# Kernel tuning notes

Measured on AMD Instinct MI355X. Metric: run time of the kernel, lower is better.

## Reference

```python
import jax, jax.numpy as jnp
import numpy as np

B, S, D, R, H = 32, 2048, 512, 4, 32  # batch, seq, input_dim, num_regimes, gru hidden

def setup_inputs() -> dict:
    key = jax.random.key(0)
    ks = jax.random.split(key, 16)
    def lin(k, fan_out, fan_in):
        s = 1.0 / np.sqrt(fan_in)
        kw, kb = jax.random.split(k)
        return (jax.random.uniform(kw, (fan_out, fan_in), jnp.float32, -s, s),
                jax.random.uniform(kb, (fan_out,), jnp.float32, -s, s))
    x = jax.random.normal(ks[0], (B, S, D), jnp.float32)
    rw1, rb1 = lin(ks[1], 128, D)
    rw2, rb2 = lin(ks[2], 64, 128)
    rw3, rb3 = lin(ks[3], R, 64)
    # experts stacked: [R, out, in]
    e1 = [lin(jax.random.fold_in(ks[4], i), 64, D) for i in range(R)]
    e2 = [lin(jax.random.fold_in(ks[5], i), 64, 64) for i in range(R)]
    ew1 = jnp.stack([w for w, _ in e1]); eb1 = jnp.stack([b for _, b in e1])
    ew2 = jnp.stack([w for w, _ in e2]); eb2 = jnp.stack([b for _, b in e2])
    sg = 1.0 / np.sqrt(H)
    gw_ih = jax.random.uniform(ks[6], (3 * H, R), jnp.float32, -sg, sg)
    gw_hh = jax.random.uniform(ks[7], (3 * H, H), jnp.float32, -sg, sg)
    gb_ih = jax.random.uniform(ks[8], (3 * H,), jnp.float32, -sg, sg)
    gb_hh = jax.random.uniform(ks[9], (3 * H,), jnp.float32, -sg, sg)
    return dict(x=x, rw1=rw1, rb1=rb1, rw2=rw2, rb2=rb2, rw3=rw3, rb3=rb3,
                ew1=ew1, eb1=eb1, ew2=ew2, eb2=eb2,
                gw_ih=gw_ih, gw_hh=gw_hh, gb_ih=gb_ih, gb_hh=gb_hh)

def reference(x, rw1, rb1, rw2, rb2, rw3, rb3, ew1, eb1, ew2, eb2, gw_ih, gw_hh, gb_ih, gb_hh):
    # --- router (dropout is identity in eval) ---
    h = jax.nn.relu(jnp.einsum('bsd,fd->bsf', x, rw1) + rb1)
    h = jax.nn.relu(jnp.einsum('bsf,gf->bsg', h, rw2) + rb2)
    probs = jax.nn.softmax(jnp.einsum('bsg,rg->bsr', h, rw3) + rb3, axis=-1)  # [B,S,R]
    # --- batched experts: one fused batched-GEMM instead of a python loop ---
    e = jax.nn.relu(jnp.einsum('bsd,red->bsre', x, ew1) + eb1)      # [B,S,R,64]
    e = jax.nn.relu(jnp.einsum('bsre,rfe->bsrf', e, ew2) + eb2)     # [B,S,R,64]
    weighted = jnp.einsum('bsrf,bsr->bsf', e, probs)                 # [B,S,64]
    # --- GRU over regime probs (pytorch gate ordering r,z,n) ---
    def step(hprev, xt):
        gi = xt @ gw_ih.T + gb_ih    # [B,3H]
        gh = hprev @ gw_hh.T + gb_hh
        ir, iz, inn = jnp.split(gi, 3, axis=-1)
        hr, hz, hn = jnp.split(gh, 3, axis=-1)
        r = jax.nn.sigmoid(ir + hr)
        z = jax.nn.sigmoid(iz + hz)
        n = jnp.tanh(inn + r * hn)
        hnew = (1.0 - z) * n + z * hprev
        return hnew, hnew
    h0 = jnp.zeros((probs.shape[0], gw_hh.shape[1]), probs.dtype)
    _, trans = jax.lax.scan(step, h0, jnp.swapaxes(probs, 0, 1))
    trans = jnp.swapaxes(trans, 0, 1)  # [B,S,H]
    uncertainty = jnp.std(probs, axis=-1, ddof=1)  # torch.std is unbiased
    return probs, weighted, trans, uncertainty
```

## Files before the change

### kernel.cpp

```cpp
#include <hip/hip_runtime.h>
#include <math.h>

#define NTOK 65536
#define TOK 64
#define NTILE 1024

__device__ __forceinline__ float xhalf_sum(float a) {
    unsigned ai = __builtin_bit_cast(unsigned, a);
    auto r = __builtin_amdgcn_permlane32_swap(ai, ai, false, false);
    return __builtin_bit_cast(float, (unsigned)r[0]) +
           __builtin_bit_cast(float, (unsigned)r[1]);
}

__global__ __launch_bounds__(256, 2) void k_router(
    const float* __restrict__ x,
    const float* __restrict__ rw1, const float* __restrict__ rb1,
    const float* __restrict__ rw2, const float* __restrict__ rb2,
    const float* __restrict__ rw3, const float* __restrict__ rb3,
    float* __restrict__ probs_out, float* __restrict__ unc_out)
{
    __shared__ float XsT[32][68];
    __shared__ float WsT[32][132];
    __shared__ float H1[64][132];
    __shared__ float H2[64][68];

    const int tid = threadIdx.x;
    const int tx = tid & 15, ty = tid >> 4;
    const long t0 = (long)blockIdx.x * TOK;

    float acc[4][8];
#pragma unroll
    for (int i = 0; i < 4; i++)
#pragma unroll
        for (int o = 0; o < 8; o++) acc[i][o] = 0.f;

    for (int kc = 0; kc < 16; kc++) {
        __syncthreads();
#pragma unroll
        for (int s = 0; s < 2; s++) {
            int id = tid + s * 256;
            int tok = id >> 3, kq = id & 7;
            float4 v = *(const float4*)&x[(t0 + tok) * 512 + kc * 32 + kq * 4];
            XsT[kq * 4 + 0][tok] = v.x; XsT[kq * 4 + 1][tok] = v.y;
            XsT[kq * 4 + 2][tok] = v.z; XsT[kq * 4 + 3][tok] = v.w;
        }
#pragma unroll
        for (int s = 0; s < 4; s++) {
            int id = tid + s * 256;
            int out = id >> 3, kq = id & 7;
            float4 v = *(const float4*)&rw1[(long)out * 512 + kc * 32 + kq * 4];
            WsT[kq * 4 + 0][out] = v.x; WsT[kq * 4 + 1][out] = v.y;
            WsT[kq * 4 + 2][out] = v.z; WsT[kq * 4 + 3][out] = v.w;
        }
        __syncthreads();
#pragma unroll
        for (int k = 0; k < 32; k++) {
            const float4 xv = *(const float4*)&XsT[k][ty * 4];
            const float4 wa = *(const float4*)&WsT[k][tx * 4];
            const float4 wb = *(const float4*)&WsT[k][64 + tx * 4];
            const float xs[4] = {xv.x, xv.y, xv.z, xv.w};
            const float ws[8] = {wa.x, wa.y, wa.z, wa.w, wb.x, wb.y, wb.z, wb.w};
#pragma unroll
            for (int i = 0; i < 4; i++)
#pragma unroll
                for (int o = 0; o < 8; o++)
                    acc[i][o] = fmaf(xs[i], ws[o], acc[i][o]);
        }
    }

#pragma unroll
    for (int o = 0; o < 8; o++) {
        const int col = (o < 4) ? (tx * 4 + o) : (64 + tx * 4 + (o - 4));
        float b = rb1[col];
#pragma unroll
        for (int i = 0; i < 4; i++) {
            float v = acc[i][o] + b;
            H1[ty * 4 + i][col] = v > 0.f ? v : 0.f;
        }
    }
    __syncthreads();

    float a2[4][4];
#pragma unroll
    for (int i = 0; i < 4; i++)
#pragma unroll
        for (int o = 0; o < 4; o++) a2[i][o] = 0.f;

    for (int k4 = 0; k4 < 32; k4++) {
        float4 hv[4], wv[4];
#pragma unroll
        for (int i = 0; i < 4; i++) hv[i] = *(const float4*)&H1[ty * 4 + i][k4 * 4];
#pragma unroll
        for (int o = 0; o < 4; o++) wv[o] = *(const float4*)&rw2[(tx * 4 + o) * 128 + k4 * 4];
#pragma unroll
        for (int i = 0; i < 4; i++)
#pragma unroll
            for (int o = 0; o < 4; o++)
                a2[i][o] += hv[i].x * wv[o].x + hv[i].y * wv[o].y +
                            hv[i].z * wv[o].z + hv[i].w * wv[o].w;
    }
#pragma unroll
    for (int o = 0; o < 4; o++) {
        float b = rb2[tx * 4 + o];
#pragma unroll
        for (int i = 0; i < 4; i++) {
            float v = a2[i][o] + b;
            H2[ty * 4 + i][tx * 4 + o] = v > 0.f ? v : 0.f;
        }
    }
    __syncthreads();

    if (tid < 64) {
        int tok = tid;
        float lg[4];
#pragma unroll
        for (int r = 0; r < 4; r++) {
            float s = rb3[r];
            for (int k4 = 0; k4 < 16; k4++) {
                float4 h = *(const float4*)&H2[tok][k4 * 4];
                float4 w = *(const float4*)&rw3[r * 64 + k4 * 4];
                s += h.x * w.x + h.y * w.y + h.z * w.z + h.w * w.w;
            }
            lg[r] = s;
        }
        float m = fmaxf(fmaxf(lg[0], lg[1]), fmaxf(lg[2], lg[3]));
        float e0 = __expf(lg[0] - m), e1 = __expf(lg[1] - m);
        float e2 = __expf(lg[2] - m), e3 = __expf(lg[3] - m);
        float inv = __builtin_amdgcn_rcpf(e0 + e1 + e2 + e3);
        float p0 = e0 * inv, p1 = e1 * inv, p2 = e2 * inv, p3 = e3 * inv;
        *(float4*)&probs_out[(t0 + tok) * 4] = make_float4(p0, p1, p2, p3);
        float mean = 0.25f * (p0 + p1 + p2 + p3);
        float d0 = p0 - mean, d1 = p1 - mean, d2 = p2 - mean, d3 = p3 - mean;
        unc_out[t0 + tok] = sqrtf((d0 * d0 + d1 * d1 + d2 * d2 + d3 * d3) * (1.f / 3.f));
    }
}

__global__ __launch_bounds__(256, 2) void k_experts_gru(
    const float* __restrict__ x,
    const float* __restrict__ ew1, const float* __restrict__ eb1,
    const float* __restrict__ ew2, const float* __restrict__ eb2,
    const float* __restrict__ probs, float* __restrict__ weighted_out,
    const float* __restrict__ gwih, const float* __restrict__ gwhh,
    const float* __restrict__ gbih, const float* __restrict__ gbhh,
    float* __restrict__ trans_out)
{
    if (blockIdx.x < 32) {
        if (threadIdx.x >= 64) return;
        const int b = blockIdx.x;
        const int l = threadIdx.x;
        const int j = l & 31, half = l >> 5;
        __shared__ __align__(16) float hS[32];

        float whh[3][16];
#pragma unroll
        for (int g = 0; g < 3; g++) {
            const float* wp = gwhh + (j + 32 * g) * 32 + half * 16;
#pragma unroll
            for (int q = 0; q < 4; q++) {
                float4 w = *(const float4*)(wp + q * 4);
                whh[g][q * 4 + 0] = w.x; whh[g][q * 4 + 1] = w.y;
                whh[g][q * 4 + 2] = w.z; whh[g][q * 4 + 3] = w.w;
            }
        }
        float wih[3][4];
#pragma unroll
        for (int g = 0; g < 3; g++) {
            float4 w = *(const float4*)&gwih[(j + 32 * g) * 4];
            wih[g][0] = w.x; wih[g][1] = w.y; wih[g][2] = w.z; wih[g][3] = w.w;
        }
        const float bR = gbih[j] + gbhh[j];
        const float bZ = gbih[j + 32] + gbhh[j + 32];
        const float bIN = gbih[j + 64], bHN = gbhh[j + 64];

        const float* pb = probs + (long)b * 2048 * 4;
        float4 p0 = *(const float4*)pb;
        float4 p1 = *(const float4*)(pb + 4);
        float hk[16];
#pragma unroll
        for (int k = 0; k < 16; k++) hk[k] = 0.f;
        float hj = 0.f;
        float* tr = trans_out + (long)b * 2048 * 32 + j;

        for (int t = 0; t < 2048; t++) {
            const int tn = (t + 2 < 2048) ? (t + 2) : 2047;
            float4 p2 = *(const float4*)(pb + tn * 4);

            float aR0 = 0.f, aR1 = 0.f, aZ0 = 0.f, aZ1 = 0.f, aN0 = 0.f, aN1 = 0.f;
#pragma unroll
            for (int k = 0; k < 16; k += 2) {
                aR0 = fmaf(whh[0][k],     hk[k],     aR0);
                aR1 = fmaf(whh[0][k + 1], hk[k + 1], aR1);
                aZ0 = fmaf(whh[1][k],     hk[k],     aZ0);
                aZ1 = fmaf(whh[1][k + 1], hk[k + 1], aZ1);
                aN0 = fmaf(whh[2][k],     hk[k],     aN0);
                aN1 = fmaf(whh[2][k + 1], hk[k + 1], aN1);
            }
            float aR = xhalf_sum(aR0 + aR1);
            float aZ = xhalf_sum(aZ0 + aZ1);
            float aN = xhalf_sum(aN0 + aN1);

            float giR = fmaf(wih[0][3], p0.w, fmaf(wih[0][2], p0.z,
                        fmaf(wih[0][1], p0.y, fmaf(wih[0][0], p0.x, bR))));
            float giZ = fmaf(wih[1][3], p0.w, fmaf(wih[1][2], p0.z,
                        fmaf(wih[1][1], p0.y, fmaf(wih[1][0], p0.x, bZ))));
            float giN = fmaf(wih[2][3], p0.w, fmaf(wih[2][2], p0.z,
                        fmaf(wih[2][1], p0.y, fmaf(wih[2][0], p0.x, bIN))));

            float r = __builtin_amdgcn_rcpf(1.f + __expf(-(giR + aR)));
            float z = __builtin_amdgcn_rcpf(1.f + __expf(-(giZ + aZ)));
            float nx = giN + r * (aN + bHN);
            float n = fmaf(2.f, __builtin_amdgcn_rcpf(1.f + __expf(-2.f * nx)), -1.f);
            hj = fmaf(z, hj - n, n);

            if (l < 32) tr[t * 32] = hj;
            hS[j] = hj;
            asm volatile("s_waitcnt lgkmcnt(0)" ::: "memory");
#pragma unroll
            for (int q = 0; q < 4; q++) {
                float4 h4 = *(const float4*)&hS[half * 16 + q * 4];
                hk[q * 4 + 0] = h4.x; hk[q * 4 + 1] = h4.y;
                hk[q * 4 + 2] = h4.z; hk[q * 4 + 3] = h4.w;
            }
            p0 = p1; p1 = p2;
        }
        return;
    }

    __shared__ float XsT[32][68];
    __shared__ float WsT[32][132];
    __shared__ float E1[64][132];
    __shared__ float pS[64][4];

    const int tid = threadIdx.x;
    const int tx = tid & 15, ty = tid >> 4;
    const long t0 = (long)(blockIdx.x - 32) * TOK;

    if (tid < 64) *(float4*)&pS[tid][0] = *(const float4*)&probs[(t0 + tid) * 4];

    float wacc[4][8];
#pragma unroll
    for (int i = 0; i < 4; i++)
#pragma unroll
        for (int o = 0; o < 8; o++) wacc[i][o] = 0.f;

    for (int g = 0; g < 2; g++) {
        float acc[4][8];
#pragma unroll
        for (int i = 0; i < 4; i++)
#pragma unroll
            for (int o = 0; o < 8; o++) acc[i][o] = 0.f;

        for (int kc = 0; kc < 16; kc++) {
            __syncthreads();
#pragma unroll
            for (int s = 0; s < 2; s++) {
                int id = tid + s * 256;
                int tok = id >> 3, kq = id & 7;
                float4 v = *(const float4*)&x[(t0 + tok) * 512 + kc * 32 + kq * 4];
                XsT[kq * 4 + 0][tok] = v.x; XsT[kq * 4 + 1][tok] = v.y;
                XsT[kq * 4 + 2][tok] = v.z; XsT[kq * 4 + 3][tok] = v.w;
            }
#pragma unroll
            for (int s = 0; s < 4; s++) {
                int id = tid + s * 256;
                int out = id >> 3, kq = id & 7;
                float4 v = *(const float4*)&ew1[(long)(g * 128 + out) * 512 + kc * 32 + kq * 4];
                WsT[kq * 4 + 0][out] = v.x; WsT[kq * 4 + 1][out] = v.y;
                WsT[kq * 4 + 2][out] = v.z; WsT[kq * 4 + 3][out] = v.w;
            }
            __syncthreads();
#pragma unroll
            for (int k = 0; k < 32; k++) {
                const float4 xv = *(const float4*)&XsT[k][ty * 4];
                const float4 wa = *(const float4*)&WsT[k][tx * 4];
                const float4 wb = *(const float4*)&WsT[k][64 + tx * 4];
                const float xs[4] = {xv.x, xv.y, xv.z, xv.w};
                const float ws[8] = {wa.x, wa.y, wa.z, wa.w, wb.x, wb.y, wb.z, wb.w};
#pragma unroll
                for (int i = 0; i < 4; i++)
#pragma unroll
                    for (int o = 0; o < 8; o++)
                        acc[i][o] = fmaf(xs[i], ws[o], acc[i][o]);
            }
        }
        __syncthreads();
#pragma unroll
        for (int o = 0; o < 8; o++) {
            const int col = (o < 4) ? (tx * 4 + o) : (64 + tx * 4 + (o - 4));
            float b = eb1[g * 128 + col];
#pragma unroll
            for (int i = 0; i < 4; i++) {
                float v = acc[i][o] + b;
                E1[ty * 4 + i][col] = v > 0.f ? v : 0.f;
            }
        }
        __syncthreads();

        const int rl = tx >> 3;
        const int fb = (tx & 7) * 8;
        const int rg = g * 2 + rl;

        float a2[4][8];
#pragma unroll
        for (int i = 0; i < 4; i++)
#pragma unroll
            for (int o = 0; o < 8; o++) a2[i][o] = 0.f;

        for (int k4 = 0; k4 < 16; k4++) {
            float4 hv[4];
#pragma unroll
            for (int i = 0; i < 4; i++)
                hv[i] = *(const float4*)&E1[ty * 4 + i][rl * 64 + k4 * 4];
#pragma unroll
            for (int o = 0; o < 8; o++) {
                float4 wv = *(const float4*)&ew2[(long)(rg * 64 + fb + o) * 64 + k4 * 4];
#pragma unroll
                for (int i = 0; i < 4; i++)
                    a2[i][o] += hv[i].x * wv.x + hv[i].y * wv.y +
                                hv[i].z * wv.z + hv[i].w * wv.w;
            }
        }
        float pr[4];
#pragma unroll
        for (int i = 0; i < 4; i++) pr[i] = pS[ty * 4 + i][rg];
#pragma unroll
        for (int o = 0; o < 8; o++) {
            float b = eb2[rg * 64 + fb + o];
#pragma unroll
            for (int i = 0; i < 4; i++) {
                float v = a2[i][o] + b;
                v = v > 0.f ? v : 0.f;
                wacc[i][o] = fmaf(pr[i], v, wacc[i][o]);
            }
        }
        __syncthreads();
    }

#pragma unroll
    for (int i = 0; i < 4; i++)
#pragma unroll
        for (int o = 0; o < 8; o++)
            wacc[i][o] += __shfl_xor(wacc[i][o], 8);

    if ((tx & 8) == 0) {
#pragma unroll
        for (int i = 0; i < 4; i++) {
            float4 v0 = make_float4(wacc[i][0], wacc[i][1], wacc[i][2], wacc[i][3]);
            float4 v1 = make_float4(wacc[i][4], wacc[i][5], wacc[i][6], wacc[i][7]);
            long base = (t0 + ty * 4 + i) * 64 + (tx & 7) * 8;
            *(float4*)&weighted_out[base] = v0;
            *(float4*)&weighted_out[base + 4] = v1;
        }
    }
}

extern "C" void kernel_launch(void* const* d_in, const int* in_sizes, int n_in,
                              void* d_out, int out_size, void* d_ws, size_t ws_size,
                              hipStream_t stream) {
    const float* x    = (const float*)d_in[0];
    const float* rw1  = (const float*)d_in[1];
    const float* rb1  = (const float*)d_in[2];
    const float* rw2  = (const float*)d_in[3];
    const float* rb2  = (const float*)d_in[4];
    const float* rw3  = (const float*)d_in[5];
    const float* rb3  = (const float*)d_in[6];
    const float* ew1  = (const float*)d_in[7];
    const float* eb1  = (const float*)d_in[8];
    const float* ew2  = (const float*)d_in[9];
    const float* eb2  = (const float*)d_in[10];
    const float* gwih = (const float*)d_in[11];
    const float* gwhh = (const float*)d_in[12];
    const float* gbih = (const float*)d_in[13];
    const float* gbhh = (const float*)d_in[14];

    float* out        = (float*)d_out;
    float* probs_o    = out;
    float* weighted_o = out + 262144;
    float* trans_o    = out + 262144 + 4194304;
    float* unc_o      = trans_o + 2097152;

    hipLaunchKernelGGL(k_router, dim3(NTILE), dim3(256), 0, stream,
                       x, rw1, rb1, rw2, rb2, rw3, rb3, probs_o, unc_o);
    hipLaunchKernelGGL(k_experts_gru, dim3(NTILE + 32), dim3(256), 0, stream,
                       x, ew1, eb1, ew2, eb2, probs_o, weighted_o,
                       gwih, gwhh, gbih, gbhh, trans_o);
}
```

Measured before the change: 829.7 us.

## Fuse router, experts and GRU into one kernel with per-tile flag handoff

Merges the router and experts/GRU kernels into a single persistent-style launch. Each token tile computes router probs, keeps them in shared memory for the expert stage, and publishes a release flag. The 32 GRU blocks spin on these flags per 64-step chunk, so the sequential recurrence can overlap the router/expert GEMMs instead of waiting for a full kernel boundary. Tiles are remapped so that early blocks cover the first chunk of every batch. Risks include spin-wait dependence on block scheduling order, plus the extra memset and shared-memory union reuse.

Result: slower. 1.139 ms (+37.2%).

```diff
diff --git a/kernel.cpp b/kernel.cpp
--- a/kernel.cpp
+++ b/kernel.cpp
@@ -1,9 +1,7 @@
 #include <hip/hip_runtime.h>
 #include <math.h>
 
-#define NTOK 65536
 #define TOK 64
-#define NTILE 1024
 
 __device__ __forceinline__ float xhalf_sum(float a) {
     unsigned ai = __builtin_bit_cast(unsigned, a);
@@ -12,21 +10,119 @@
            __builtin_bit_cast(float, (unsigned)r[1]);
 }
 
-__global__ __launch_bounds__(256, 2) void k_router(
+__global__ __launch_bounds__(256, 2) void k_fused(
     const float* __restrict__ x,
     const float* __restrict__ rw1, const float* __restrict__ rb1,
     const float* __restrict__ rw2, const float* __restrict__ rb2,
     const float* __restrict__ rw3, const float* __restrict__ rb3,
-    float* __restrict__ probs_out, float* __restrict__ unc_out)
+    const float* __restrict__ ew1, const float* __restrict__ eb1,
+    const float* __restrict__ ew2, const float* __restrict__ eb2,
+    const float* __restrict__ gwih, const float* __restrict__ gwhh,
+    const float* __restrict__ gbih, const float* __restrict__ gbhh,
+    float* __restrict__ probs_out, float* __restrict__ unc_out,
+    float* __restrict__ weighted_out, float* __restrict__ trans_out,
+    unsigned* __restrict__ flags)
 {
-    __shared__ float XsT[32][68];
-    __shared__ float WsT[32][132];
-    __shared__ float H1[64][132];
-    __shared__ float H2[64][68];
+    __shared__ float H1E1[64][132];
+    union SU { struct { float XsT[32][68]; float WsT[32][132]; } s; float H2[64][68]; };
+    __shared__ SU u;
+    __shared__ float pS[64][4];
+    __shared__ __align__(16) float hS[32];
+
+    if (blockIdx.x < 32) {
+        if (threadIdx.x >= 64) return;
+        const int b = blockIdx.x;
+        const int l = threadIdx.x;
+        const int j = l & 31, half = l >> 5;
+
+        float whh[3][16];
+#pragma unroll
+        for (int g = 0; g < 3; g++) {
+            const float* wp = gwhh + (j + 32 * g) * 32 + half * 16;
+#pragma unroll
+            for (int qq = 0; qq < 4; qq++) {
+                float4 w = *(const float4*)(wp + qq * 4);
+                whh[g][qq * 4 + 0] = w.x; whh[g][qq * 4 + 1] = w.y;
+                whh[g][qq * 4 + 2] = w.z; whh[g][qq * 4 + 3] = w.w;
+            }
+        }
+        float wih[3][4];
+#pragma unroll
+        for (int g = 0; g < 3; g++) {
+            float4 w = *(const float4*)&gwih[(j + 32 * g) * 4];
+            wih[g][0] = w.x; wih[g][1] = w.y; wih[g][2] = w.z; wih[g][3] = w.w;
+        }
+        const float bR = gbih[j] + gbhh[j];
+        const float bZ = gbih[j + 32] + gbhh[j + 32];
+        const float bIN = gbih[j + 64], bHN = gbhh[j + 64];
+
+        float hk[16];
+#pragma unroll
+        for (int k = 0; k < 16; k++) hk[k] = 0.f;
+        float hj = 0.f;
+        float* tr = trans_out + (long)b * 2048 * 32 + j;
+        const unsigned* flg = flags + b * 32;
+
+        for (int blk = 0; blk < 32; ++blk) {
+            while (__hip_atomic_load(&flg[blk], __ATOMIC_ACQUIRE,
+                                     __HIP_MEMORY_SCOPE_AGENT) == 0u) {
+                __builtin_amdgcn_s_sleep(8);
+            }
+            const float* pt = probs_out + ((long)b * 2048 + blk * 64) * 4;
+            float4 p0 = *(const float4*)pt;
+            float4 p1 = *(const float4*)(pt + 4);
+
+            for (int t = 0; t < 64; t++) {
+                const int tn = (t + 2 < 64) ? (t + 2) : 63;
+                float4 p2 = *(const float4*)(pt + tn * 4);
+
+                float aR0 = 0.f, aR1 = 0.f, aZ0 = 0.f, aZ1 = 0.f, aN0 = 0.f, aN1 = 0.f;
+#pragma unroll
+                for (int k = 0; k < 16; k += 2) {
+                    aR0 = fmaf(whh[0][k],     hk[k],     aR0);
+                    aR1 = fmaf(whh[0][k + 1], hk[k + 1], aR1);
+                    aZ0 = fmaf(whh[1][k],     hk[k],     aZ0);
+                    aZ1 = fmaf(whh[1][k + 1], hk[k + 1], aZ1);
+                    aN0 = fmaf(whh[2][k],     hk[k],     aN0);
+                    aN1 = fmaf(whh[2][k + 1], hk[k + 1], aN1);
+                }
+                float aR = xhalf_sum(aR0 + aR1);
+                float aZ = xhalf_sum(aZ0 + aZ1);
+                float aN = xhalf_sum(aN0 + aN1);
+
+                float giR = fmaf(wih[0][3], p0.w, fmaf(wih[0][2], p0.z,
+                            fmaf(wih[0][1], p0.y, fmaf(wih[0][0], p0.x, bR))));
+                float giZ = fmaf(wih[1][3], p0.w, fmaf(wih[1][2], p0.z,
+                            fmaf(wih[1][1], p0.y, fmaf(wih[1][0], p0.x, bZ))));
+                float giN = fmaf(wih[2][3], p0.w, fmaf(wih[2][2], p0.z,
+                            fmaf(wih[2][1], p0.y, fmaf(wih[2][0], p0.x, bIN))));
+
+                float r = __builtin_amdgcn_rcpf(1.f + __expf(-(giR + aR)));
+                float z = __builtin_amdgcn_rcpf(1.f + __expf(-(giZ + aZ)));
+                float nx = giN + r * (aN + bHN);
+                float n = fmaf(2.f, __builtin_amdgcn_rcpf(1.f + __expf(-2.f * nx)), -1.f);
+                hj = fmaf(z, hj - n, n);
+
+                if (l < 32) tr[(blk * 64 + t) * 32] = hj;
+                hS[j] = hj;
+#pragma unroll
+                for (int qq = 0; qq < 4; qq++) {
+                    float4 h4 = *(const float4*)&hS[half * 16 + qq * 4];
+                    hk[qq * 4 + 0] = h4.x; hk[qq * 4 + 1] = h4.y;
+                    hk[qq * 4 + 2] = h4.z; hk[qq * 4 + 3] = h4.w;
+                }
+                p0 = p1; p1 = p2;
+            }
+        }
+        return;
+    }
+
+    const int q = blockIdx.x - 32;
+    const int tile = (q & 31) * 32 + (q >> 5);
+    const long t0 = (long)tile * TOK;
 
     const int tid = threadIdx.x;
     const int tx = tid & 15, ty = tid >> 4;
-    const long t0 = (long)blockIdx.x * TOK;
 
     float acc[4][8];
 #pragma unroll
@@ -41,23 +137,23 @@
             int id = tid + s * 256;
             int tok = id >> 3, kq = id & 7;
             float4 v = *(const float4*)&x[(t0 + tok) * 512 + kc * 32 + kq * 4];
-            XsT[kq * 4 + 0][tok] = v.x; XsT[kq * 4 + 1][tok] = v.y;
-            XsT[kq * 4 + 2][tok] = v.z; XsT[kq * 4 + 3][tok] = v.w;
+            u.s.XsT[kq * 4 + 0][tok] = v.x; u.s.XsT[kq * 4 + 1][tok] = v.y;
+            u.s.XsT[kq * 4 + 2][tok] = v.z; u.s.XsT[kq * 4 + 3][tok] = v.w;
         }
 #pragma unroll
         for (int s = 0; s < 4; s++) {
             int id = tid + s * 256;
             int out = id >> 3, kq = id & 7;
             float4 v = *(const float4*)&rw1[(long)out * 512 + kc * 32 + kq * 4];
-            WsT[kq * 4 + 0][out] = v.x; WsT[kq * 4 + 1][out] = v.y;
-            WsT[kq * 4 + 2][out] = v.z; WsT[kq * 4 + 3][out] = v.w;
+            u.s.WsT[kq * 4 + 0][out] = v.x; u.s.WsT[kq * 4 + 1][out] = v.y;
+            u.s.WsT[kq * 4 + 2][out] = v.z; u.s.WsT[kq * 4 + 3][out] = v.w;
         }
         __syncthreads();
 #pragma unroll
         for (int k = 0; k < 32; k++) {
-            const float4 xv = *(const float4*)&XsT[k][ty * 4];
-            const float4 wa = *(const float4*)&WsT[k][tx * 4];
-            const float4 wb = *(const float4*)&WsT[k][64 + tx * 4];
+            const float4 xv = *(const float4*)&u.s.XsT[k][ty * 4];
+            const float4 wa = *(const float4*)&u.s.WsT[k][tx * 4];
+            const float4 wb = *(const float4*)&u.s.WsT[k][64 + tx * 4];
             const float xs[4] = {xv.x, xv.y, xv.z, xv.w};
             const float ws[8] = {wa.x, wa.y, wa.z, wa.w, wb.x, wb.y, wb.z, wb.w};
 #pragma unroll
@@ -75,37 +171,37 @@
 #pragma unroll
         for (int i = 0; i < 4; i++) {
             float v = acc[i][o] + b;
-            H1[ty * 4 + i][col] = v > 0.f ? v : 0.f;
+            H1E1[ty * 4 + i][col] = v > 0.f ? v : 0.f;
         }
     }
     __syncthreads();
 
-    float a2[4][4];
+    float a2r[4][4];
 #pragma unroll
     for (int i = 0; i < 4; i++)
 #pragma unroll
-        for (int o = 0; o < 4; o++) a2[i][o] = 0.f;
+        for (int o = 0; o < 4; o++) a2r[i][o] = 0.f;
 
     for (int k4 = 0; k4 < 32; k4++) {
         float4 hv[4], wv[4];
 #pragma unroll
-        for (int i = 0; i < 4; i++) hv[i] = *(const float4*)&H1[ty * 4 + i][k4 * 4];
+        for (int i = 0; i < 4; i++) hv[i] = *(const float4*)&H1E1[ty * 4 + i][k4 * 4];
 #pragma unroll
         for (int o = 0; o < 4; o++) wv[o] = *(const float4*)&rw2[(tx * 4 + o) * 128 + k4 * 4];
 #pragma unroll
         for (int i = 0; i < 4; i++)
 #pragma unroll
             for (int o = 0; o < 4; o++)
-                a2[i][o] += hv[i].x * wv[o].x + hv[i].y * wv[o].y +
-                            hv[i].z * wv[o].z + hv[i].w * wv[o].w;
+                a2r[i][o] += hv[i].x * wv[o].x + hv[i].y * wv[o].y +
+                             hv[i].z * wv[o].z + hv[i].w * wv[o].w;
     }
 #pragma unroll
     for (int o = 0; o < 4; o++) {
         float b = rb2[tx * 4 + o];
 #pragma unroll
         for (int i = 0; i < 4; i++) {
-            float v = a2[i][o] + b;
-            H2[ty * 4 + i][tx * 4 + o] = v > 0.f ? v : 0.f;
+            float v = a2r[i][o] + b;
+            u.H2[ty * 4 + i][tx * 4 + o] = v > 0.f ? v : 0.f;
         }
     }
     __syncthreads();
@@ -117,7 +213,7 @@
         for (int r = 0; r < 4; r++) {
             float s = rb3[r];
             for (int k4 = 0; k4 < 16; k4++) {
-                float4 h = *(const float4*)&H2[tok][k4 * 4];
+                float4 h = *(const float4*)&u.H2[tok][k4 * 4];
                 float4 w = *(const float4*)&rw3[r * 64 + k4 * 4];
                 s += h.x * w.x + h.y * w.y + h.z * w.z + h.w * w.w;
             }
@@ -129,113 +225,16 @@
         float inv = __builtin_amdgcn_rcpf(e0 + e1 + e2 + e3);
         float p0 = e0 * inv, p1 = e1 * inv, p2 = e2 * inv, p3 = e3 * inv;
         *(float4*)&probs_out[(t0 + tok) * 4] = make_float4(p0, p1, p2, p3);
+        pS[tok][0] = p0; pS[tok][1] = p1; pS[tok][2] = p2; pS[tok][3] = p3;
         float mean = 0.25f * (p0 + p1 + p2 + p3);
         float d0 = p0 - mean, d1 = p1 - mean, d2 = p2 - mean, d3 = p3 - mean;
         unc_out[t0 + tok] = sqrtf((d0 * d0 + d1 * d1 + d2 * d2 + d3 * d3) * (1.f / 3.f));
     }
-}
-
-__global__ __launch_bounds__(256, 2) void k_experts_gru(
-    const float* __restrict__ x,
-    const float* __restrict__ ew1, const float* __restrict__ eb1,
-    const float* __restrict__ ew2, const float* __restrict__ eb2,
-    const float* __restrict__ probs, float* __restrict__ weighted_out,
-    const float* __restrict__ gwih, const float* __restrict__ gwhh,
-    const float* __restrict__ gbih, const float* __restrict__ gbhh,
-    float* __restrict__ trans_out)
-{
-    if (blockIdx.x < 32) {
-        if (threadIdx.x >= 64) return;
-        const int b = blockIdx.x;
-        const int l = threadIdx.x;
-        const int j = l & 31, half = l >> 5;
-        __shared__ __align__(16) float hS[32];
-
-        float whh[3][16];
-#pragma unroll
-        for (int g = 0; g < 3; g++) {
-            const float* wp = gwhh + (j + 32 * g) * 32 + half * 16;
-#pragma unroll
-            for (int q = 0; q < 4; q++) {
-                float4 w = *(const float4*)(wp + q * 4);
-                whh[g][q * 4 + 0] = w.x; whh[g][q * 4 + 1] = w.y;
-                whh[g][q * 4 + 2] = w.z; whh[g][q * 4 + 3] = w.w;
-            }
-        }
-        float wih[3][4];
-#pragma unroll
-        for (int g = 0; g < 3; g++) {
-            float4 w = *(const float4*)&gwih[(j + 32 * g) * 4];
-            wih[g][0] = w.x; wih[g][1] = w.y; wih[g][2] = w.z; wih[g][3] = w.w;
-        }
-        const float bR = gbih[j] + gbhh[j];
-        const float bZ = gbih[j + 32] + gbhh[j + 32];
-        const float bIN = gbih[j + 64], bHN = gbhh[j + 64];
-
-        const float* pb = probs + (long)b * 2048 * 4;
-        float4 p0 = *(const float4*)pb;
-        float4 p1 = *(const float4*)(pb + 4);
-        float hk[16];
-#pragma unroll
-        for (int k = 0; k < 16; k++) hk[k] = 0.f;
-        float hj = 0.f;
-        float* tr = trans_out + (long)b * 2048 * 32 + j;
-
-        for (int t = 0; t < 2048; t++) {
-            const int tn = (t + 2 < 2048) ? (t + 2) : 2047;
-            float4 p2 = *(const float4*)(pb + tn * 4);
-
-            float aR0 = 0.f, aR1 = 0.f, aZ0 = 0.f, aZ1 = 0.f, aN0 = 0.f, aN1 = 0.f;
-#pragma unroll
-            for (int k = 0; k < 16; k += 2) {
-                aR0 = fmaf(whh[0][k],     hk[k],     aR0);
-                aR1 = fmaf(whh[0][k + 1], hk[k + 1], aR1);
-                aZ0 = fmaf(whh[1][k],     hk[k],     aZ0);
-                aZ1 = fmaf(whh[1][k + 1], hk[k + 1], aZ1);
-                aN0 = fmaf(whh[2][k],     hk[k],     aN0);
-                aN1 = fmaf(whh[2][k + 1], hk[k + 1], aN1);
-            }
-            float aR = xhalf_sum(aR0 + aR1);
-            float aZ = xhalf_sum(aZ0 + aZ1);
-            float aN = xhalf_sum(aN0 + aN1);
-
-            float giR = fmaf(wih[0][3], p0.w, fmaf(wih[0][2], p0.z,
-                        fmaf(wih[0][1], p0.y, fmaf(wih[0][0], p0.x, bR))));
-            float giZ = fmaf(wih[1][3], p0.w, fmaf(wih[1][2], p0.z,
-                        fmaf(wih[1][1], p0.y, fmaf(wih[1][0], p0.x, bZ))));
-            float giN = fmaf(wih[2][3], p0.w, fmaf(wih[2][2], p0.z,
-                        fmaf(wih[2][1], p0.y, fmaf(wih[2][0], p0.x, bIN))));
-
-            float r = __builtin_amdgcn_rcpf(1.f + __expf(-(giR + aR)));
-            float z = __builtin_amdgcn_rcpf(1.f + __expf(-(giZ + aZ)));
-            float nx = giN + r * (aN + bHN);
-            float n = fmaf(2.f, __builtin_amdgcn_rcpf(1.f + __expf(-2.f * nx)), -1.f);
-            hj = fmaf(z, hj - n, n);
-
-            if (l < 32) tr[t * 32] = hj;
-            hS[j] = hj;
-            asm volatile("s_waitcnt lgkmcnt(0)" ::: "memory");
-#pragma unroll
-            for (int q = 0; q < 4; q++) {
-                float4 h4 = *(const float4*)&hS[half * 16 + q * 4];
-                hk[q * 4 + 0] = h4.x; hk[q * 4 + 1] = h4.y;
-                hk[q * 4 + 2] = h4.z; hk[q * 4 + 3] = h4.w;
-            }
-            p0 = p1; p1 = p2;
-        }
-        return;
-    }
-
-    __shared__ float XsT[32][68];
-    __shared__ float WsT[32][132];
-    __shared__ float E1[64][132];
-    __shared__ float pS[64][4];
-
-    const int tid = threadIdx.x;
-    const int tx = tid & 15, ty = tid >> 4;
-    const long t0 = (long)(blockIdx.x - 32) * TOK;
-
-    if (tid < 64) *(float4*)&pS[tid][0] = *(const float4*)&probs[(t0 + tid) * 4];
+    __syncthreads();
+
+    if (tid == 0)
+        __hip_atomic_store(&flags[tile], 1u, __ATOMIC_RELEASE,
+                           __HIP_MEMORY_SCOPE_AGENT);
 
     float wacc[4][8];
 #pragma unroll
@@ -244,11 +243,11 @@
         for (int o = 0; o < 8; o++) wacc[i][o] = 0.f;
 
     for (int g = 0; g < 2; g++) {
-        float acc[4][8];
+        float eacc[4][8];
 #pragma unroll
         for (int i = 0; i < 4; i++)
 #pragma unroll
-            for (int o = 0; o < 8; o++) acc[i][o] = 0.f;
+            for (int o = 0; o < 8; o++) eacc[i][o] = 0.f;
 
         for (int kc = 0; kc < 16; kc++) {
             __syncthreads();
@@ -257,30 +256,30 @@
                 int id = tid + s * 256;
                 int tok = id >> 3, kq = id & 7;
                 float4 v = *(const float4*)&x[(t0 + tok) * 512 + kc * 32 + kq * 4];
-                XsT[kq * 4 + 0][tok] = v.x; XsT[kq * 4 + 1][tok] = v.y;
-                XsT[kq * 4 + 2][tok] = v.z; XsT[kq * 4 + 3][tok] = v.w;
+                u.s.XsT[kq * 4 + 0][tok] = v.x; u.s.XsT[kq * 4 + 1][tok] = v.y;
+                u.s.XsT[kq * 4 + 2][tok] = v.z; u.s.XsT[kq * 4 + 3][tok] = v.w;
             }
 #pragma unroll
             for (int s = 0; s < 4; s++) {
                 int id = tid + s * 256;
                 int out = id >> 3, kq = id & 7;
                 float4 v = *(const float4*)&ew1[(long)(g * 128 + out) * 512 + kc * 32 + kq * 4];
-                WsT[kq * 4 + 0][out] = v.x; WsT[kq * 4 + 1][out] = v.y;
-                WsT[kq * 4 + 2][out] = v.z; WsT[kq * 4 + 3][out] = v.w;
+                u.s.WsT[kq * 4 + 0][out] = v.x; u.s.WsT[kq * 4 + 1][out] = v.y;
+                u.s.WsT[kq * 4 + 2][out] = v.z; u.s.WsT[kq * 4 + 3][out] = v.w;
             }
             __syncthreads();
 #pragma unroll
             for (int k = 0; k < 32; k++) {
-                const float4 xv = *(const float4*)&XsT[k][ty * 4];
-                const float4 wa = *(const float4*)&WsT[k][tx * 4];
-                const float4 wb = *(const float4*)&WsT[k][64 + tx * 4];
+                const float4 xv = *(const float4*)&u.s.XsT[k][ty * 4];
+                const float4 wa = *(const float4*)&u.s.WsT[k][tx * 4];
+                const float4 wb = *(const float4*)&u.s.WsT[k][64 + tx * 4];
                 const float xs[4] = {xv.x, xv.y, xv.z, xv.w};
                 const float ws[8] = {wa.x, wa.y, wa.z, wa.w, wb.x, wb.y, wb.z, wb.w};
 #pragma unroll
                 for (int i = 0; i < 4; i++)
 #pragma unroll
                     for (int o = 0; o < 8; o++)
-                        acc[i][o] = fmaf(xs[i], ws[o], acc[i][o]);
+                        eacc[i][o] = fmaf(xs[i], ws[o], eacc[i][o]);
             }
         }
         __syncthreads();
@@ -290,8 +289,8 @@
             float b = eb1[g * 128 + col];
 #pragma unroll
             for (int i = 0; i < 4; i++) {
-                float v = acc[i][o] + b;
-                E1[ty * 4 + i][col] = v > 0.f ? v : 0.f;
+                float v = eacc[i][o] + b;
+                H1E1[ty * 4 + i][col] = v > 0.f ? v : 0.f;
             }
         }
         __syncthreads();
@@ -310,7 +309,7 @@
             float4 hv[4];
 #pragma unroll
             for (int i = 0; i < 4; i++)
-                hv[i] = *(const float4*)&E1[ty * 4 + i][rl * 64 + k4 * 4];
+                hv[i] = *(const float4*)&H1E1[ty * 4 + i][rl * 64 + k4 * 4];
 #pragma unroll
             for (int o = 0; o < 8; o++) {
                 float4 wv = *(const float4*)&ew2[(long)(rg * 64 + fb + o) * 64 + k4 * 4];
@@ -379,9 +378,12 @@
     float* trans_o    = out + 262144 + 4194304;
     float* unc_o      = trans_o + 2097152;
 
-    hipLaunchKernelGGL(k_router, dim3(NTILE), dim3(256), 0, stream,
-                       x, rw1, rb1, rw2, rb2, rw3, rb3, probs_o, unc_o);
-    hipLaunchKernelGGL(k_experts_gru, dim3(NTILE + 32), dim3(256), 0, stream,
-                       x, ew1, eb1, ew2, eb2, probs_o, weighted_o,
-                       gwih, gwhh, gbih, gbhh, trans_o);
+    unsigned* flags = (unsigned*)d_ws;
+    hipMemsetAsync(d_ws, 0, 1024 * sizeof(unsigned), stream);
+
+    hipLaunchKernelGGL(k_fused, dim3(1056), dim3(256), 0, stream,
+                       x, rw1, rb1, rw2, rb2, rw3, rb3,
+                       ew1, eb1, ew2, eb2,
+                       gwih, gwhh, gbih, gbhh,
+                       probs_o, unc_o, weighted_o, trans_o, flags);
 }
```
